# Optimization experiments

Measured on AMD Instinct MI355X. Metric: run time of the kernel, lower is better.

Reference implementation:

```python
import jax, jax.numpy as jnp
import numpy as np

B, T, D, N = 8, 2048, 1024, 256


def setup_inputs() -> dict:
    key = jax.random.key(0)
    ks = jax.random.split(key, 6)
    sD = 1.0 / np.sqrt(D)
    sN = 1.0 / np.sqrt(N)
    return {
        "x": jax.random.normal(ks[0], (B, T, D), dtype=jnp.float32),
        "Wa": jax.random.normal(ks[1], (D, N), dtype=jnp.float32) * sD,
        "ba": jnp.zeros((N,), jnp.float32),
        "Wb": jax.random.normal(ks[2], (D, N), dtype=jnp.float32) * sD,
        "bb": jnp.zeros((N,), jnp.float32),
        "Wc": jax.random.normal(ks[3], (D, N), dtype=jnp.float32) * sD,
        "bc": jnp.zeros((N,), jnp.float32),
        "Wd": jax.random.normal(ks[4], (D, D), dtype=jnp.float32) * sD,
        "bd": jnp.zeros((D,), jnp.float32),
        "Wy": jax.random.normal(ks[5], (N, D), dtype=jnp.float32) * sN,
        "by": jnp.zeros((D,), jnp.float32),
    }


def reference(x, Wa, ba, Wb, bb, Wc, bc, Wd, bd, Wy, by):
    # Precompute all input-dependent gates/projections in batched GEMMs.
    a = jax.nn.sigmoid(jnp.einsum("btd,dn->btn", x, Wa) + ba)  # (B,T,N)
    b = jnp.einsum("btd,dn->btn", x, Wb) + bb                   # (B,T,N)
    c = jnp.tanh(jnp.einsum("btd,dn->btn", x, Wc) + bc)          # (B,T,N)
    d = jnp.einsum("btd,de->bte", x, Wd) + bd                    # (B,T,D)

    # Sequential linear-gated recurrence: s_t = a_t*s_{t-1} + (1-a_t)*b_t
    def step(s, abc):
        at, bt, ct = abc
        s = at * s + (1.0 - at) * bt
        return s, ct * s

    aT = jnp.swapaxes(a, 0, 1)  # (T,B,N)
    bT = jnp.swapaxes(b, 0, 1)
    cT = jnp.swapaxes(c, 0, 1)
    s0 = jnp.zeros((x.shape[0], Wa.shape[1]), x.dtype)
    _, csT = jax.lax.scan(step, s0, (aT, bT, cT))  # (T,B,N)
    cs = jnp.swapaxes(csT, 0, 1)                    # (B,T,N)

    # Output projection applied once over the full sequence.
    y = jnp.einsum("btn,nd->btd", cs, Wy) + by + d  # (B,T,D)
    return y
```

## Files before the change

### kernel.cpp

```cpp
#include <hip/hip_runtime.h>
#include <hip/hip_bf16.h>

typedef unsigned short u16;
typedef __attribute__((ext_vector_type(8))) short bf16x8;
typedef __attribute__((ext_vector_type(4))) float f32x4;

#define AS1 __attribute__((address_space(1)))
#define AS3 __attribute__((address_space(3)))

#define Bx 8
#define Tt 2048
#define Dd 1024
#define Nn 256
#define Mm (Bx*Tt)
#define CHAINS (Bx*Nn)
#define NCH 32
#define TC 64
#define NCOMB 1792

#define WS_NEED 130809856u

__device__ __forceinline__ u16 f2bf(float f) {
  union { float f; unsigned u; } v; v.f = f;
  unsigned u = v.u;
  u += 0x7fffu + ((u >> 16) & 1u);
  return (u16)(u >> 16);
}

__device__ __forceinline__ float bf2f(u16 h) {
  union { unsigned u; float f; } v; v.u = ((unsigned)h) << 16;
  return v.f;
}

__device__ __forceinline__ void gload_lds16(const void* g, void* l) {
  __builtin_amdgcn_global_load_lds((AS1 void*)(g), (AS3 void*)(l), 16, 0, 0);
}

__global__ void cvt_x_kernel(const float* __restrict__ x, u16* __restrict__ xb) {
  int i = blockIdx.x * blockDim.x + threadIdx.x;
  float4 v = ((const float4*)x)[i];
  unsigned lo = (unsigned)f2bf(v.x) | ((unsigned)f2bf(v.y) << 16);
  unsigned hi = (unsigned)f2bf(v.z) | ((unsigned)f2bf(v.w) << 16);
  ((uint2*)xb)[i] = make_uint2(lo, hi);
}

__global__ void pack_w_kernel(const float* __restrict__ Wa, const float* __restrict__ Wb,
                              const float* __restrict__ Wc, const float* __restrict__ Wd,
                              const float* __restrict__ Wy,
                              u16* __restrict__ Wcomb, u16* __restrict__ Wyt) {
  __shared__ float tile[32][33];
  int z = blockIdx.z;
  const float* src; u16* dst; int R, C, dld;
  if (z < 3)       { src = (z==0?Wa:(z==1?Wb:Wc)); dst = Wcomb + (size_t)z*256*1024; R=1024; C=256;  dld=1024; }
  else if (z == 3) { src = Wd; dst = Wcomb + (size_t)768*1024; R=1024; C=1024; dld=1024; }
  else             { src = Wy; dst = Wyt; R=256;  C=1024; dld=256;  }
  int c0 = blockIdx.x * 32, r0 = blockIdx.y * 32;
  if (c0 >= C || r0 >= R) return;
  int tx = threadIdx.x & 31, ty = threadIdx.x >> 5;
  #pragma unroll
  for (int i = 0; i < 32; i += 8)
    tile[ty + i][tx] = src[(size_t)(r0 + ty + i)*C + (c0 + tx)];
  __syncthreads();
  #pragma unroll
  for (int i = 0; i < 32; i += 8) {
    int c = c0 + ty + i, r = r0 + tx;
    dst[(size_t)c*dld + r] = f2bf(tile[tx][ty + i]);
  }
}

template<int EPI>
__global__ __launch_bounds__(256, 3) void gemm_bt_kernel(
    const u16* __restrict__ A, const u16* __restrict__ Bt, int K,
    float* __restrict__ outA, float* __restrict__ outO, u16* __restrict__ dtmp,
    const float* __restrict__ b0, const float* __restrict__ b1,
    const float* __restrict__ b2, const float* __restrict__ b3) {
  __shared__ u16 ldsA[128*64];
  __shared__ u16 ldsB[128*64];
  const int tid = threadIdx.x;
  const int lane = tid & 63, wid = tid >> 6;
  const int wr = wid >> 1, wc = wid & 1;
  const int m0 = blockIdx.y * 128, n0 = blockIdx.x * 128;

  f32x4 acc[4][4] = {};

  const int srow = lane >> 3;
  const int sq   = (lane & 7) ^ srow;
  const char* Ab = (const char*)A;
  const char* Bb = (const char*)Bt;

  const int kq  = lane >> 4;
  const int swz = lane & 7;
  const int arow = wr*64 + (lane & 15);
  const int brow = wc*64 + (lane & 15);

  for (int k0 = 0; k0 < K; k0 += 64) {
    #pragma unroll
    for (int i = 0; i < 4; ++i) {
      int g = wid*4 + i;
      int r = g*8 + srow;
      gload_lds16(Ab + ((size_t)(m0 + r)*K + k0 + sq*8)*2, (char*)ldsA + g*1024);
      gload_lds16(Bb + ((size_t)(n0 + r)*K + k0 + sq*8)*2, (char*)ldsB + g*1024);
    }
    __syncthreads();
    #pragma unroll
    for (int kk = 0; kk < 2; ++kk) {
      const int q = ((kk*4 + kq) ^ swz) * 8;
      bf16x8 af[4], bfr[4];
      #pragma unroll
      for (int mi = 0; mi < 4; ++mi)
        af[mi]  = *(const bf16x8*)&ldsA[(arow + mi*16)*64 + q];
      #pragma unroll
      for (int ni = 0; ni < 4; ++ni)
        bfr[ni] = *(const bf16x8*)&ldsB[(brow + ni*16)*64 + q];
      #pragma unroll
      for (int mi = 0; mi < 4; ++mi)
        #pragma unroll
        for (int ni = 0; ni < 4; ++ni)
          acc[mi][ni] = __builtin_amdgcn_mfma_f32_16x16x32_bf16(af[mi], bfr[ni], acc[mi][ni], 0, 0, 0);
    }
    __syncthreads();
  }

  const int crow = m0 + wr*64 + (lane >> 4)*4;
  const int ccol = wc*64 + (lane & 15);
  #pragma unroll
  for (int mi = 0; mi < 4; ++mi) {
    #pragma unroll
    for (int ni = 0; ni < 4; ++ni) {
      int coln = n0 + ccol + ni*16;
      #pragma unroll
      for (int r = 0; r < 4; ++r) {
        int row = crow + mi*16 + r;
        float v = acc[mi][ni][r];
        if (EPI == 0) {
          if (n0 < 768) {
            int seg = coln >> 8, cn = coln & 255;
            if (seg == 0)      v = 1.f / (1.f + __expf(-(v + b0[cn])));
            else if (seg == 1) v = v + b1[cn];
            else               v = tanhf(v + b2[cn]);
            outA[(size_t)row*768 + coln] = v;
          } else {
            int col = coln - 768;
            if (dtmp) dtmp[(size_t)row*1024 + col] = f2bf(v + b3[col]);
            else      outO[(size_t)row*1024 + col] = v + b3[col];
          }
        } else {
          const size_t o = (size_t)row*1024 + coln;
          if (dtmp) outO[o] = v + b0[coln] + bf2f(dtmp[o]);
          else      outO[o] = outO[o] + v + b0[coln];
        }
      }
    }
  }
}

__global__ void scanA_kernel(const float* __restrict__ abc,
                             float* __restrict__ Asum, float* __restrict__ Usum) {
  int idx = blockIdx.x * blockDim.x + threadIdx.x;
  int chain = idx & (CHAINS - 1);
  int ch = idx >> 11;
  int bb = chain >> 8, n = chain & 255;
  const float* base = abc + (size_t)(bb*Tt + ch*TC) * 768;
  float A = 1.f, U = 0.f;
  for (int t = 0; t < TC; ++t) {
    float a = base[(size_t)t*768 + n];
    float b = base[(size_t)t*768 + 256 + n];
    U = a*U + (1.f - a)*b;
    A *= a;
  }
  Asum[idx] = A; Usum[idx] = U;
}

__global__ void scanB_kernel(const float* __restrict__ Asum, const float* __restrict__ Usum,
                             float* __restrict__ Spre) {
  int chain = blockIdx.x * blockDim.x + threadIdx.x;
  float s = 0.f;
  for (int ch = 0; ch < NCH; ++ch) {
    int i = (ch << 11) + chain;
    Spre[i] = s;
    s = Asum[i]*s + Usum[i];
  }
}

__global__ void scanC_kernel(const float* __restrict__ abc, const float* __restrict__ Spre,
                             u16* __restrict__ cs) {
  int idx = blockIdx.x * blockDim.x + threadIdx.x;
  int chain = idx & (CHAINS - 1);
  int ch = idx >> 11;
  int bb = chain >> 8, n = chain & 255;
  const float* base = abc + (size_t)(bb*Tt + ch*TC) * 768;
  u16* csb = cs + (size_t)(bb*Tt + ch*TC) * 256 + n;
  float s = Spre[idx];
  for (int t = 0; t < TC; ++t) {
    float a = base[(size_t)t*768 + n];
    float b = base[(size_t)t*768 + 256 + n];
    float c = base[(size_t)t*768 + 512 + n];
    s = a*s + (1.f - a)*b;
    csb[(size_t)t*256] = f2bf(c*s);
  }
}

extern "C" void kernel_launch(void* const* d_in, const int* in_sizes, int n_in,
                              void* d_out, int out_size, void* d_ws, size_t ws_size,
                              hipStream_t stream) {
  const float* x  = (const float*)d_in[0];
  const float* Wa = (const float*)d_in[1];
  const float* ba = (const float*)d_in[2];
  const float* Wb = (const float*)d_in[3];
  const float* bb = (const float*)d_in[4];
  const float* Wc = (const float*)d_in[5];
  const float* bc = (const float*)d_in[6];
  const float* Wd = (const float*)d_in[7];
  const float* bd = (const float*)d_in[8];
  const float* Wy = (const float*)d_in[9];
  const float* by = (const float*)d_in[10];
  float* out = (float*)d_out;
  char* ws = (char*)d_ws;

  u16*  xb    = (u16*) (ws + 0);
  u16*  Wcomb = (u16*) (ws + 33554432);
  u16*  Wyt   = (u16*) (ws + 37224448);
  float* abc  = (float*)(ws + 37748736);
  u16*  cs    = (u16*) (ws + 88080384);
  float* Asum = (float*)(ws + 96468992);
  float* Usum = (float*)(ws + 96731136);
  float* Spre = (float*)(ws + 96993280);
  u16*  dtmp  = (ws_size >= WS_NEED) ? (u16*)(ws + 97255424) : nullptr;

  cvt_x_kernel<<<Mm*Dd/4/256, 256, 0, stream>>>(x, xb);
  pack_w_kernel<<<dim3(32, 32, 5), 256, 0, stream>>>(Wa, Wb, Wc, Wd, Wy, Wcomb, Wyt);
  gemm_bt_kernel<0><<<dim3(NCOMB/128, Mm/128), 256, 0, stream>>>(
      xb, Wcomb, Dd, abc, out, dtmp, ba, bb, bc, bd);
  scanA_kernel<<<CHAINS*NCH/256, 256, 0, stream>>>(abc, Asum, Usum);
  scanB_kernel<<<CHAINS/256, 256, 0, stream>>>(Asum, Usum, Spre);
  scanC_kernel<<<CHAINS*NCH/256, 256, 0, stream>>>(abc, Spre, cs);
  gemm_bt_kernel<2><<<dim3(Dd/128, Mm/128), 256, 0, stream>>>(
      cs, Wyt, Nn, nullptr, out, dtmp, by, nullptr, nullptr, nullptr);
}
```

Before: 174.5 us.

## Double-buffer LDS tiles in GEMM to overlap global loads with MFMA

The GEMM kernel now uses two LDS buffers per operand. Each iteration reads the current tile's fragments into registers, issues the global-to-LDS loads for the next tile, then runs the MFMAs at raised wave priority. This aims to hide global load latency behind compute and cut one barrier per iteration. In exchange it doubles LDS use and register pressure, so launch bounds drop from 3 to 2 blocks per CU, which lowers occupancy.

```diff
diff --git a/kernel.cpp b/kernel.cpp
--- a/kernel.cpp
+++ b/kernel.cpp
@@ -69,17 +69,18 @@
 }
 
 template<int EPI>
-__global__ __launch_bounds__(256, 3) void gemm_bt_kernel(
+__global__ __launch_bounds__(256, 2) void gemm_bt_kernel(
     const u16* __restrict__ A, const u16* __restrict__ Bt, int K,
     float* __restrict__ outA, float* __restrict__ outO, u16* __restrict__ dtmp,
     const float* __restrict__ b0, const float* __restrict__ b1,
     const float* __restrict__ b2, const float* __restrict__ b3) {
-  __shared__ u16 ldsA[128*64];
-  __shared__ u16 ldsB[128*64];
+  __shared__ u16 ldsA[2*128*64];
+  __shared__ u16 ldsB[2*128*64];
   const int tid = threadIdx.x;
   const int lane = tid & 63, wid = tid >> 6;
   const int wr = wid >> 1, wc = wid & 1;
   const int m0 = blockIdx.y * 128, n0 = blockIdx.x * 128;
+  const int NT = K >> 6;
 
   f32x4 acc[4][4] = {};
 
@@ -88,36 +89,53 @@
   const char* Ab = (const char*)A;
   const char* Bb = (const char*)Bt;
 
+  auto stage = [&](int b, int t) {
+    const int k0 = t << 6;
+    #pragma unroll
+    for (int i = 0; i < 4; ++i) {
+      int g = wid*4 + i;
+      int r = g*8 + srow;
+      gload_lds16(Ab + ((size_t)(m0 + r)*K + k0 + sq*8)*2, (char*)ldsA + b*16384 + g*1024);
+      gload_lds16(Bb + ((size_t)(n0 + r)*K + k0 + sq*8)*2, (char*)ldsB + b*16384 + g*1024);
+    }
+  };
+
   const int kq  = lane >> 4;
   const int swz = lane & 7;
   const int arow = wr*64 + (lane & 15);
   const int brow = wc*64 + (lane & 15);
 
-  for (int k0 = 0; k0 < K; k0 += 64) {
-    #pragma unroll
-    for (int i = 0; i < 4; ++i) {
-      int g = wid*4 + i;
-      int r = g*8 + srow;
-      gload_lds16(Ab + ((size_t)(m0 + r)*K + k0 + sq*8)*2, (char*)ldsA + g*1024);
-      gload_lds16(Bb + ((size_t)(n0 + r)*K + k0 + sq*8)*2, (char*)ldsB + g*1024);
-    }
-    __syncthreads();
+  stage(0, 0);
+  __syncthreads();
+
+  for (int t = 0; t < NT; ++t) {
+    const int cur = t & 1;
+    const int cb  = cur * 8192;
+
+    bf16x8 af[2][4], bfr[2][4];
     #pragma unroll
     for (int kk = 0; kk < 2; ++kk) {
       const int q = ((kk*4 + kq) ^ swz) * 8;
-      bf16x8 af[4], bfr[4];
       #pragma unroll
       for (int mi = 0; mi < 4; ++mi)
-        af[mi]  = *(const bf16x8*)&ldsA[(arow + mi*16)*64 + q];
+        af[kk][mi]  = *(const bf16x8*)&ldsA[cb + (arow + mi*16)*64 + q];
       #pragma unroll
       for (int ni = 0; ni < 4; ++ni)
-        bfr[ni] = *(const bf16x8*)&ldsB[(brow + ni*16)*64 + q];
+        bfr[kk][ni] = *(const bf16x8*)&ldsB[cb + (brow + ni*16)*64 + q];
+    }
+
+    if (t + 1 < NT) stage(cur ^ 1, t + 1);
+
+    __builtin_amdgcn_s_setprio(1);
+    #pragma unroll
+    for (int kk = 0; kk < 2; ++kk)
       #pragma unroll
       for (int mi = 0; mi < 4; ++mi)
         #pragma unroll
         for (int ni = 0; ni < 4; ++ni)
-          acc[mi][ni] = __builtin_amdgcn_mfma_f32_16x16x32_bf16(af[mi], bfr[ni], acc[mi][ni], 0, 0, 0);
-    }
+          acc[mi][ni] = __builtin_amdgcn_mfma_f32_16x16x32_bf16(af[kk][mi], bfr[kk][ni], acc[mi][ni], 0, 0, 0);
+    __builtin_amdgcn_s_setprio(0);
+
     __syncthreads();
   }
 
```

Result: slower. 205.1 us (+17.5%).
